# Performance work log

Hardware: AMD Instinct MI355X
Metric: run time of the kernel (lower is better)

The kernel has to match this reference:

```python
import jax, jax.numpy as jnp
import numpy as np

N = 50000
E = 800000
IN_DIM = 256
HID = 64
HEADS = 6
OUT_DIM = 32
NEG_SLOPE = 0.2


def gat_conv(x, src, dst, W, att_src, att_dst, bias, heads, ch, n_nodes):
    """PyG GATConv (eval mode): lin proj, per-edge LeakyReLU attention,
    segment softmax over destination neighborhoods, scatter-add aggregate.
    src/dst already include self-loops. Returns [n_nodes, heads, ch]."""
    h = (x @ W).reshape(n_nodes, heads, ch)            # [N,H,C]
    a_src = jnp.sum(h * att_src, axis=-1)              # [N,H]
    a_dst = jnp.sum(h * att_dst, axis=-1)              # [N,H]
    e = jax.nn.leaky_relu(a_src[src] + a_dst[dst], NEG_SLOPE)   # [E,H]
    m = jax.ops.segment_max(e, dst, num_segments=n_nodes)       # [N,H]
    ex = jnp.exp(e - m[dst])                                    # [E,H]
    denom = jax.ops.segment_sum(ex, dst, num_segments=n_nodes)  # [N,H]
    alpha = ex / denom[dst]                                     # [E,H]
    out = jax.ops.segment_sum(h[src] * alpha[:, :, None], dst, num_segments=n_nodes)
    return out + bias.reshape(1, heads, ch)


def setup_inputs() -> dict:
    key = jax.random.key(0)
    ks = jax.random.split(key, 10)
    x = jax.random.normal(ks[0], (N, IN_DIM), dtype=jnp.float32)
    edge_index = jax.random.randint(ks[1], (2, E), 0, N, dtype=jnp.int64)
    s1 = 1.0 / np.sqrt(IN_DIM)
    W1 = jax.random.normal(ks[2], (IN_DIM, HEADS * HID), dtype=jnp.float32) * s1
    att_src1 = jax.random.normal(ks[3], (1, HEADS, HID), dtype=jnp.float32) * 0.1
    att_dst1 = jax.random.normal(ks[4], (1, HEADS, HID), dtype=jnp.float32) * 0.1
    b1 = jnp.zeros((HEADS * HID,), dtype=jnp.float32)
    s2 = 1.0 / np.sqrt(HEADS * HID)
    W2 = jax.random.normal(ks[5], (HEADS * HID, OUT_DIM), dtype=jnp.float32) * s2
    att_src2 = jax.random.normal(ks[6], (1, 1, OUT_DIM), dtype=jnp.float32) * 0.1
    att_dst2 = jax.random.normal(ks[7], (1, 1, OUT_DIM), dtype=jnp.float32) * 0.1
    b2 = jnp.zeros((OUT_DIM,), dtype=jnp.float32)
    return {"x": x, "edge_index": edge_index, "W1": W1, "att_src1": att_src1,
            "att_dst1": att_dst1, "b1": b1, "W2": W2, "att_src2": att_src2,
            "att_dst2": att_dst2, "b2": b2}


def reference(x, edge_index, W1, att_src1, att_dst1, b1, W2, att_src2, att_dst2, b2):
    # PyG GATConv default add_self_loops=True
    loops = jnp.arange(N, dtype=edge_index.dtype)
    src = jnp.concatenate([edge_index[0], loops])
    dst = jnp.concatenate([edge_index[1], loops])
    h1 = gat_conv(x, src, dst, W1, att_src1, att_dst1, b1, HEADS, HID, N)
    h1 = jax.nn.relu(h1.reshape(N, HEADS * HID))  # concat=True, then ReLU; dropout = identity (eval)
    h2 = gat_conv(h1, src, dst, W2, att_src2, att_dst2, b2, 1, OUT_DIM, N)
    return h2.reshape(N, OUT_DIM)  # concat=False with 1 head == mean == squeeze
```

## Files before the change

### kernel.cpp

```cpp
#include <hip/hip_runtime.h>
#include <hip/hip_bf16.h>

#define NN 50000
#define EE 800000
#define IN_DIM 256
#define HID 64
#define HEADS 6
#define D1 384
#define OUT_DIM 32
#define NEG_SLOPE 0.2f
#define CAP 128
#define NBLK 196

typedef unsigned int uint32;
typedef unsigned short ushort_t;
typedef short short8 __attribute__((ext_vector_type(8)));
typedef float f32x4 __attribute__((ext_vector_type(4)));
typedef float f32x2 __attribute__((ext_vector_type(2)));
typedef ushort_t ushort8 __attribute__((ext_vector_type(8)));

__device__ __forceinline__ ushort_t f2bf(float f) {
    uint32 u = __builtin_bit_cast(uint32, f);
    u += 0x7fffu + ((u >> 16) & 1u);
    return (ushort_t)(u >> 16);
}
__device__ __forceinline__ float bf2f(ushort_t s) {
    uint32 u = ((uint32)s) << 16;
    return __builtin_bit_cast(float, u);
}
__device__ __forceinline__ float lo16(uint32 d) { return __builtin_bit_cast(float, d << 16); }
__device__ __forceinline__ float hi16(uint32 d) { return __builtin_bit_cast(float, d & 0xffff0000u); }


__global__ void hist_kernel(const int* __restrict__ dst, int* __restrict__ deg) {
    int i = blockIdx.x * 256 + threadIdx.x;
    if (i < EE) atomicAdd(&deg[dst[i]], 1);
}

__global__ __launch_bounds__(256) void scan1_kernel(const int* __restrict__ deg,
                                                    int* __restrict__ blockSums) {
    int t = threadIdx.x;
    int i = blockIdx.x * 256 + t;
    int v = (i < NN) ? (deg[i] + 1) : 0;
#pragma unroll
    for (int o = 32; o; o >>= 1) v += __shfl_xor(v, o);
    __shared__ int ws[4];
    if ((t & 63) == 0) ws[t >> 6] = v;
    __syncthreads();
    if (t == 0) blockSums[blockIdx.x] = ws[0] + ws[1] + ws[2] + ws[3];
}

__global__ __launch_bounds__(256) void scan2_kernel(const int* __restrict__ blockSums,
                                                    int* __restrict__ blockPrefix,
                                                    int* __restrict__ offsets) {
    int t = threadIdx.x;
    int lane = t & 63, w = t >> 6;
    int v = (t < NBLK) ? blockSums[t] : 0;
    int x = v;
#pragma unroll
    for (int o = 1; o < 64; o <<= 1) {
        int y = __shfl_up(x, o);
        if (lane >= o) x += y;
    }
    __shared__ int ws[4];
    if (lane == 63) ws[w] = x;
    __syncthreads();
    int wpre = 0;
#pragma unroll
    for (int k = 0; k < 4; ++k) if (k < w) wpre += ws[k];
    int incl = x + wpre;
    if (t < NBLK) blockPrefix[t] = incl - v;
    if (t == NBLK - 1) offsets[NN] = incl;
}

__global__ __launch_bounds__(256) void scan3_kernel(const int* __restrict__ deg,
                                                    const int* __restrict__ blockPrefix,
                                                    int* __restrict__ offsets,
                                                    int* __restrict__ cursor) {
    int t = threadIdx.x;
    int i = blockIdx.x * 256 + t;
    int lane = t & 63, w = t >> 6;
    int v = (i < NN) ? (deg[i] + 1) : 0;
    int x = v;
#pragma unroll
    for (int o = 1; o < 64; o <<= 1) {
        int y = __shfl_up(x, o);
        if (lane >= o) x += y;
    }
    __shared__ int ws[4];
    if (lane == 63) ws[w] = x;
    __syncthreads();
    int wpre = 0;
#pragma unroll
    for (int k = 0; k < 4; ++k) if (k < w) wpre += ws[k];
    int excl = x + wpre - v + blockPrefix[blockIdx.x];
    if (i < NN) { offsets[i] = excl; cursor[i] = excl; }
}

__global__ void scatter_kernel(const int* __restrict__ src, const int* __restrict__ dst,
                               int* __restrict__ cursor, int* __restrict__ srcIdx) {
    int i = blockIdx.x * 256 + threadIdx.x;
    if (i >= EE + NN) return;
    int s, d;
    if (i < EE) { s = src[i]; d = dst[i]; }
    else        { s = i - EE; d = s; }
    int pos = atomicAdd(&cursor[d], 1);
    srcIdx[pos] = s;
}


__global__ __launch_bounds__(256) void w1t_kernel(const float* __restrict__ W1,
                                                  ushort_t* __restrict__ W1Tb) {
    __shared__ float tile[32][33];
    int tx = threadIdx.x & 31, ty = threadIdx.x >> 5;
    int n0 = blockIdx.x * 32;
    int k0 = blockIdx.y * 32;
#pragma unroll
    for (int i = 0; i < 4; ++i)
        tile[ty + i * 8][tx] = W1[(k0 + ty + i * 8) * D1 + n0 + tx];
    __syncthreads();
#pragma unroll
    for (int i = 0; i < 4; ++i)
        W1Tb[(n0 + ty + i * 8) * IN_DIM + k0 + tx] = f2bf(tile[tx][ty + i * 8]);
}

__global__ __launch_bounds__(256) void w2t_kernel(const float* __restrict__ W2,
                                                  ushort_t* __restrict__ W2Tb) {
    int idx = blockIdx.x * 256 + threadIdx.x;
    if (idx < D1 * OUT_DIM) {
        int k = idx >> 5, n = idx & 31;
        W2Tb[n * D1 + k] = f2bf(W2[idx]);
    }
}


#define G1_BM 128
#define G1_BK 64

__global__ __launch_bounds__(512) void gemm1_kernel(const float* __restrict__ A,
                                                    const ushort_t* __restrict__ Bt,
                                                    const float* __restrict__ att_src,
                                                    const float* __restrict__ att_dst,
                                                    ushort_t* __restrict__ Cb,
                                                    float* __restrict__ a_src1,
                                                    float* __restrict__ a_dst1) {
    __shared__ __align__(16) ushort_t As[G1_BM][G1_BK];
    __shared__ __align__(16) ushort_t Bs[D1][G1_BK];
    __shared__ float redS[G1_BM][8];
    __shared__ float redD[G1_BM][8];
    int t = threadIdx.x;
    int m0 = blockIdx.x * G1_BM;
    int wid = t >> 6, lane = t & 63;
    int rg = wid >> 2, cg = wid & 3;
    int lrow = lane & 15, lk = lane >> 4;
    f32x4 acc[4][6] = {};
    for (int k0 = 0; k0 < IN_DIM; k0 += G1_BK) {
        {
            int r = t >> 3, c = t & 7;
#pragma unroll
            for (int p = 0; p < 2; ++p) {
                int row = p * 64 + r;
                int gr = m0 + row;
                float4 v0 = make_float4(0.f, 0.f, 0.f, 0.f), v1 = v0;
                if (gr < NN) {
                    const float* g = &A[(size_t)gr * IN_DIM + k0 + c * 8];
                    v0 = *reinterpret_cast<const float4*>(g);
                    v1 = *reinterpret_cast<const float4*>(g + 4);
                }
                ushort8 u;
                u[0] = f2bf(v0.x); u[1] = f2bf(v0.y); u[2] = f2bf(v0.z); u[3] = f2bf(v0.w);
                u[4] = f2bf(v1.x); u[5] = f2bf(v1.y); u[6] = f2bf(v1.z); u[7] = f2bf(v1.w);
                *reinterpret_cast<ushort8*>(&As[row][(c ^ (row & 7)) * 8]) = u;
            }
        }
        {
            int r = t >> 3, c = t & 7;
#pragma unroll
            for (int p = 0; p < 6; ++p) {
                int row = p * 64 + r;
                ushort8 u = *reinterpret_cast<const ushort8*>(&Bt[row * IN_DIM + k0 + c * 8]);
                *reinterpret_cast<ushort8*>(&Bs[row][(c ^ (row & 7)) * 8]) = u;
            }
        }
        __syncthreads();
#pragma unroll
        for (int kk = 0; kk < G1_BK; kk += 32) {
            int ckb = (kk >> 3) + lk;
            short8 af[4];
#pragma unroll
            for (int fm = 0; fm < 4; ++fm) {
                int m = rg * 64 + fm * 16 + lrow;
                af[fm] = *reinterpret_cast<const short8*>(&As[m][(ckb ^ (m & 7)) * 8]);
            }
#pragma unroll
            for (int fn = 0; fn < 6; ++fn) {
                int n = cg * 96 + fn * 16 + lrow;
                short8 bfv = *reinterpret_cast<const short8*>(&Bs[n][(ckb ^ (n & 7)) * 8]);
#pragma unroll
                for (int fm = 0; fm < 4; ++fm)
                    acc[fm][fn] = __builtin_amdgcn_mfma_f32_16x16x32_bf16(af[fm], bfv, acc[fm][fn], 0, 0, 0);
            }
        }
        __syncthreads();
    }
    float atS[6], atD[6];
#pragma unroll
    for (int fn = 0; fn < 6; ++fn) {
        int col = cg * 96 + fn * 16 + lrow;
        atS[fn] = att_src[col];
        atD[fn] = att_dst[col];
    }
    int split = (cg & 1) ? 2 : 4;
#pragma unroll
    for (int fm = 0; fm < 4; ++fm) {
#pragma unroll
        for (int r = 0; r < 4; ++r) {
            int rowl = rg * 64 + fm * 16 + lk * 4 + r;
            int row = m0 + rowl;
            float vsA = 0.f, vsB = 0.f, vdA = 0.f, vdB = 0.f;
#pragma unroll
            for (int fn = 0; fn < 6; ++fn) {
                float v = acc[fm][fn][r];
                if (fn < split) { vsA += v * atS[fn]; vdA += v * atD[fn]; }
                else            { vsB += v * atS[fn]; vdB += v * atD[fn]; }
            }
#pragma unroll
            for (int o = 8; o; o >>= 1) {
                vsA += __shfl_xor(vsA, o); vsB += __shfl_xor(vsB, o);
                vdA += __shfl_xor(vdA, o); vdB += __shfl_xor(vdB, o);
            }
            if (lrow == 0) {
                redS[rowl][cg * 2 + 0] = vsA; redS[rowl][cg * 2 + 1] = vsB;
                redD[rowl][cg * 2 + 0] = vdA; redD[rowl][cg * 2 + 1] = vdB;
            }
            if (row < NN) {
#pragma unroll
                for (int fn = 0; fn < 6; ++fn) {
                    int col = cg * 96 + fn * 16 + lrow;
                    Cb[(size_t)row * D1 + col] = f2bf(acc[fm][fn][r]);
                }
            }
        }
    }
    __syncthreads();
    if (t < G1_BM) {
        int row = m0 + t;
        if (row < NN) {
            float s0 = redS[t][0], s1 = redS[t][1] + redS[t][2], s2 = redS[t][3];
            float s3 = redS[t][4], s4 = redS[t][5] + redS[t][6], s5 = redS[t][7];
            float d0 = redD[t][0], d1 = redD[t][1] + redD[t][2], d2 = redD[t][3];
            float d3 = redD[t][4], d4 = redD[t][5] + redD[t][6], d5 = redD[t][7];
            float* ps = &a_src1[(size_t)row * HEADS];
            float* pd = &a_dst1[(size_t)row * HEADS];
            ps[0] = s0; ps[1] = s1; ps[2] = s2; ps[3] = s3; ps[4] = s4; ps[5] = s5;
            pd[0] = d0; pd[1] = d1; pd[2] = d2; pd[3] = d3; pd[4] = d4; pd[5] = d5;
        }
    }
}


__global__ __launch_bounds__(256, 4) void agg1_kernel(const uint32* __restrict__ H1d,
                                                      const float* __restrict__ a_src,
                                                      const float* __restrict__ a_dst,
                                                      const int* __restrict__ offsets,
                                                      const int* __restrict__ srcIdx,
                                                      const float* __restrict__ b1,
                                                      uint32* __restrict__ out1d) {
    __shared__ float pl[4][HEADS][CAP + 1];
    __shared__ int   sl[4][CAP];
    int w = threadIdx.x >> 6, lane = threadIdx.x & 63;
    int hb = lane >> 5;
    int n = blockIdx.x * 4 + w;
    const float2* asv = (const float2*)a_src;
    float ad[HEADS];
#pragma unroll
    for (int h = 0; h < HEADS; ++h) ad[h] = a_dst[n * HEADS + h];
    float ldn[HEADS] = {0.f, 0.f, 0.f, 0.f, 0.f, 0.f};
    float acc[6] = {0.f, 0.f, 0.f, 0.f, 0.f, 0.f};
    int beg = offsets[n], end = offsets[n + 1];
    for (int cbeg = beg; cbeg < end; cbeg += CAP) {
        int L = end - cbeg; if (L > CAP) L = CAP;
        for (int tI = lane; tI < L; tI += 64) {
            int s = srcIdx[cbeg + tI];
            sl[w][tI] = s;
            float2 e0 = asv[s * 3 + 0];
            float2 e1 = asv[s * 3 + 1];
            float2 e2 = asv[s * 3 + 2];
            float ev[6] = {e0.x, e0.y, e1.x, e1.y, e2.x, e2.y};
#pragma unroll
            for (int h = 0; h < HEADS; ++h) {
                float e = ev[h] + ad[h];
                e = e > 0.f ? e : NEG_SLOPE * e;
                float p = __expf(e);
                pl[w][h][tI] = p;
                ldn[h] += p;
            }
        }
        int j = 0;
        for (; j + 4 <= L; j += 4) {
            int s0 = sl[w][j], s1 = sl[w][j + 1], s2 = sl[w][j + 2], s3 = sl[w][j + 3];
            const uint32* h0 = H1d + (size_t)s0 * 192 + lane;
            const uint32* h1 = H1d + (size_t)s1 * 192 + lane;
            const uint32* h2 = H1d + (size_t)s2 * 192 + lane;
            const uint32* h3 = H1d + (size_t)s3 * 192 + lane;
            uint32 a0 = h0[0], a1 = h0[64], a2 = h0[128];
            uint32 b0 = h1[0], b1v_ = h1[64], b2 = h1[128];
            uint32 c0 = h2[0], c1 = h2[64], c2 = h2[128];
            uint32 d0 = h3[0], d1 = h3[64], d2 = h3[128];
            float p00 = pl[w][hb][j],     p01 = pl[w][2 + hb][j],     p02 = pl[w][4 + hb][j];
            float p10 = pl[w][hb][j + 1], p11 = pl[w][2 + hb][j + 1], p12 = pl[w][4 + hb][j + 1];
            float p20 = pl[w][hb][j + 2], p21 = pl[w][2 + hb][j + 2], p22 = pl[w][4 + hb][j + 2];
            float p30 = pl[w][hb][j + 3], p31 = pl[w][2 + hb][j + 3], p32 = pl[w][4 + hb][j + 3];
            acc[0] += p00 * lo16(a0); acc[1] += p00 * hi16(a0);
            acc[2] += p01 * lo16(a1); acc[3] += p01 * hi16(a1);
            acc[4] += p02 * lo16(a2); acc[5] += p02 * hi16(a2);
            acc[0] += p10 * lo16(b0); acc[1] += p10 * hi16(b0);
            acc[2] += p11 * lo16(b1v_); acc[3] += p11 * hi16(b1v_);
            acc[4] += p12 * lo16(b2); acc[5] += p12 * hi16(b2);
            acc[0] += p20 * lo16(c0); acc[1] += p20 * hi16(c0);
            acc[2] += p21 * lo16(c1); acc[3] += p21 * hi16(c1);
            acc[4] += p22 * lo16(c2); acc[5] += p22 * hi16(c2);
            acc[0] += p30 * lo16(d0); acc[1] += p30 * hi16(d0);
            acc[2] += p31 * lo16(d1); acc[3] += p31 * hi16(d1);
            acc[4] += p32 * lo16(d2); acc[5] += p32 * hi16(d2);
        }
        for (; j < L; ++j) {
            int s0 = sl[w][j];
            const uint32* h0 = H1d + (size_t)s0 * 192 + lane;
            uint32 x0 = h0[0], x1 = h0[64], x2 = h0[128];
            float p0 = pl[w][hb][j], p1 = pl[w][2 + hb][j], p2 = pl[w][4 + hb][j];
            acc[0] += p0 * lo16(x0); acc[1] += p0 * hi16(x0);
            acc[2] += p1 * lo16(x1); acc[3] += p1 * hi16(x1);
            acc[4] += p2 * lo16(x2); acc[5] += p2 * hi16(x2);
        }
    }
#pragma unroll
    for (int h = 0; h < HEADS; ++h) {
#pragma unroll
        for (int o = 32; o; o >>= 1) ldn[h] += __shfl_xor(ldn[h], o);
    }
    float dsel[3];
#pragma unroll
    for (int k = 0; k < 3; ++k) dsel[k] = hb ? ldn[2 * k + 1] : ldn[2 * k];
    const float2* b1v = (const float2*)b1;
#pragma unroll
    for (int k = 0; k < 3; ++k) {
        float2 bb = b1v[k * 64 + lane];
        float v0 = fmaxf(acc[2 * k]     / dsel[k] + bb.x, 0.f);
        float v1 = fmaxf(acc[2 * k + 1] / dsel[k] + bb.y, 0.f);
        uint32 pk = (uint32)f2bf(v0) | ((uint32)f2bf(v1) << 16);
        __builtin_nontemporal_store(pk, &out1d[(size_t)n * 192 + k * 64 + lane]);
    }
}


#define G2_ROWS 256

__global__ __launch_bounds__(256) void gemm2_kernel(const ushort_t* __restrict__ Xb,
                                                    const ushort_t* __restrict__ W2Tb,
                                                    const float* __restrict__ att_src2,
                                                    const float* __restrict__ att_dst2,
                                                    ushort_t* __restrict__ H2b,
                                                    float* __restrict__ a_src2,
                                                    float* __restrict__ a_dst2) {
    __shared__ __align__(16) ushort_t Ws[OUT_DIM][D1];
    __shared__ __align__(16) ushort_t Xs[G2_ROWS][64];
    int t = threadIdx.x;
    int wid = t >> 6, lane = t & 63;
    int lrow = lane & 15, lk = lane >> 4;
    int m0 = blockIdx.x * G2_ROWS;
#pragma unroll
    for (int p = 0; p < 6; ++p) {
        int chunk = p * 256 + t;
        int nr = chunk / 48, c = chunk % 48;
        ushort8 u = *reinterpret_cast<const ushort8*>(&W2Tb[nr * D1 + c * 8]);
        int span = c >> 3, cc = c & 7;
        *reinterpret_cast<ushort8*>(&Ws[nr][(cc ^ (nr & 7)) * 8 + span * 64]) = u;
    }
    f32x4 acc[4][2] = {};
    for (int kc = 0; kc < 6; ++kc) {
        int k0 = kc * 64;
        {
            int r = t >> 3, c = t & 7;
#pragma unroll
            for (int p = 0; p < 8; ++p) {
                int row = p * 32 + r;
                int gr = m0 + row;
                ushort8 u = {0, 0, 0, 0, 0, 0, 0, 0};
                if (gr < NN) u = *reinterpret_cast<const ushort8*>(&Xb[(size_t)gr * D1 + k0 + c * 8]);
                *reinterpret_cast<ushort8*>(&Xs[row][(c ^ (row & 7)) * 8]) = u;
            }
        }
        __syncthreads();
#pragma unroll
        for (int kk = 0; kk < 64; kk += 32) {
            int ckb = (kk >> 3) + lk;
            short8 af[4];
#pragma unroll
            for (int fm = 0; fm < 4; ++fm) {
                int mm = wid * 64 + fm * 16 + lrow;
                af[fm] = *reinterpret_cast<const short8*>(&Xs[mm][(ckb ^ (mm & 7)) * 8]);
            }
#pragma unroll
            for (int fn = 0; fn < 2; ++fn) {
                int nn2 = fn * 16 + lrow;
                short8 bfv = *reinterpret_cast<const short8*>(&Ws[nn2][(ckb ^ (nn2 & 7)) * 8 + kc * 64]);
#pragma unroll
                for (int fm = 0; fm < 4; ++fm)
                    acc[fm][fn] = __builtin_amdgcn_mfma_f32_16x16x32_bf16(af[fm], bfv, acc[fm][fn], 0, 0, 0);
            }
        }
        __syncthreads();
    }
    float as2a = att_src2[lrow], as2b = att_src2[16 + lrow];
    float ad2a = att_dst2[lrow], ad2b = att_dst2[16 + lrow];
#pragma unroll
    for (int fm = 0; fm < 4; ++fm) {
#pragma unroll
        for (int r = 0; r < 4; ++r) {
            int row = m0 + wid * 64 + fm * 16 + lk * 4 + r;
            float h0 = acc[fm][0][r], h1 = acc[fm][1][r];
            float vs = h0 * as2a + h1 * as2b;
            float vd = h0 * ad2a + h1 * ad2b;
#pragma unroll
            for (int o = 8; o; o >>= 1) {
                vs += __shfl_xor(vs, o);
                vd += __shfl_xor(vd, o);
            }
            if (row < NN) {
                H2b[(size_t)row * OUT_DIM + lrow]      = f2bf(h0);
                H2b[(size_t)row * OUT_DIM + 16 + lrow] = f2bf(h1);
                if (lrow == 0) { a_src2[row] = vs; a_dst2[row] = vd; }
            }
        }
    }
}


__global__ __launch_bounds__(256, 4) void agg2_kernel(const ushort_t* __restrict__ H2b,
                                                      const float* __restrict__ a_src,
                                                      const float* __restrict__ a_dst,
                                                      const int* __restrict__ offsets,
                                                      const int* __restrict__ srcIdx,
                                                      const float* __restrict__ b2,
                                                      float* __restrict__ out) {
    __shared__ float pl[4][CAP];
    __shared__ int   sl[4][CAP];
    int w = threadIdx.x >> 6, lane = threadIdx.x & 63;
    int n = blockIdx.x * 4 + w;
    int q = lane & 15, par = lane >> 4;
    const uint32* H2d = (const uint32*)H2b;
    float ad = a_dst[n];
    float ldn = 0.f, ax = 0.f, ay = 0.f;
    int beg = offsets[n], end = offsets[n + 1];
    for (int cbeg = beg; cbeg < end; cbeg += CAP) {
        int L = end - cbeg; if (L > CAP) L = CAP;
        for (int tI = lane; tI < L; tI += 64) {
            int s = srcIdx[cbeg + tI];
            sl[w][tI] = s;
            float e = a_src[s] + ad;
            e = e > 0.f ? e : NEG_SLOPE * e;
            float p = __expf(e);
            pl[w][tI] = p;
            ldn += p;
        }
        int j = 0;
        for (; j + 8 <= L; j += 8) {
            int s0 = sl[w][j + par], s1 = sl[w][j + 4 + par];
            float p0 = pl[w][j + par], p1 = pl[w][j + 4 + par];
            uint32 d0 = H2d[(size_t)s0 * 16 + q];
            uint32 d1 = H2d[(size_t)s1 * 16 + q];
            ax += p0 * lo16(d0) + p1 * lo16(d1);
            ay += p0 * hi16(d0) + p1 * hi16(d1);
        }
        for (; j < L; j += 4) {
            int jj = j + par;
            if (jj < L) {
                int s = sl[w][jj];
                float p = pl[w][jj];
                uint32 d = H2d[(size_t)s * 16 + q];
                ax += p * lo16(d);
                ay += p * hi16(d);
            }
        }
    }
#pragma unroll
    for (int o = 32; o; o >>= 1) ldn += __shfl_xor(ldn, o);
    ax += __shfl_xor(ax, 16); ax += __shfl_xor(ax, 32);
    ay += __shfl_xor(ay, 16); ay += __shfl_xor(ay, 32);
    if (lane < 16) {
        float2 bb = ((const float2*)b2)[q];
        f32x2 o;
        o[0] = ax / ldn + bb.x;
        o[1] = ay / ldn + bb.y;
        __builtin_nontemporal_store(o, (f32x2*)&out[(size_t)n * 32 + q * 2]);
    }
}


static inline size_t align256(size_t x) { return (x + 255) & ~size_t(255); }

extern "C" void kernel_launch(void* const* d_in, const int* in_sizes, int n_in,
                              void* d_out, int out_size, void* d_ws, size_t ws_size,
                              hipStream_t stream) {
    const float* x        = (const float*)d_in[0];
    const int*   ei       = (const int*)d_in[1];
    const float* W1       = (const float*)d_in[2];
    const float* att_src1 = (const float*)d_in[3];
    const float* att_dst1 = (const float*)d_in[4];
    const float* b1       = (const float*)d_in[5];
    const float* W2       = (const float*)d_in[6];
    const float* att_src2 = (const float*)d_in[7];
    const float* att_dst2 = (const float*)d_in[8];
    const float* b2       = (const float*)d_in[9];
    float* out = (float*)d_out;

    const int* e_src = ei;
    const int* e_dst = ei + EE;

    char* p = (char*)d_ws;
    ushort_t* H1b   = (ushort_t*)p; p += align256(sizeof(ushort_t) * (size_t)NN * D1);
    ushort_t* OUT1b = (ushort_t*)p; p += align256(sizeof(ushort_t) * (size_t)NN * D1);
    ushort_t* H2b   = (ushort_t*)p; p += align256(sizeof(ushort_t) * (size_t)NN * OUT_DIM);
    ushort_t* W1Tb  = (ushort_t*)p; p += align256(sizeof(ushort_t) * D1 * IN_DIM);
    ushort_t* W2Tb  = (ushort_t*)p; p += align256(sizeof(ushort_t) * D1 * OUT_DIM);
    float* AS1  = (float*)p; p += align256(sizeof(float) * NN * HEADS);
    float* AD1  = (float*)p; p += align256(sizeof(float) * NN * HEADS);
    float* AS2  = (float*)p; p += align256(sizeof(float) * NN);
    float* AD2  = (float*)p; p += align256(sizeof(float) * NN);
    int*   DEG  = (int*)p;   p += align256(sizeof(int) * NN);
    int*   OFF  = (int*)p;   p += align256(sizeof(int) * (NN + 1));
    int*   CUR  = (int*)p;   p += align256(sizeof(int) * NN);
    int*   BSUM = (int*)p;   p += align256(sizeof(int) * NBLK);
    int*   BPRE = (int*)p;   p += align256(sizeof(int) * NBLK);
    int*   SIDX = (int*)p;   p += align256(sizeof(int) * (EE + NN));

    (void)hipMemsetAsync(DEG, 0, sizeof(int) * NN, stream);
    w1t_kernel<<<dim3(D1 / 32, IN_DIM / 32), 256, 0, stream>>>(W1, W1Tb);
    w2t_kernel<<<48, 256, 0, stream>>>(W2, W2Tb);
    hist_kernel<<<(EE + 255) / 256, 256, 0, stream>>>(e_dst, DEG);
    scan1_kernel<<<NBLK, 256, 0, stream>>>(DEG, BSUM);
    scan2_kernel<<<1, 256, 0, stream>>>(BSUM, BPRE, OFF);
    scan3_kernel<<<NBLK, 256, 0, stream>>>(DEG, BPRE, OFF, CUR);
    scatter_kernel<<<(EE + NN + 255) / 256, 256, 0, stream>>>(e_src, e_dst, CUR, SIDX);

    gemm1_kernel<<<(NN + G1_BM - 1) / G1_BM, 512, 0, stream>>>(x, W1Tb, att_src1, att_dst1, H1b, AS1, AD1);
    agg1_kernel<<<NN / 4, 256, 0, stream>>>((const uint32*)H1b, AS1, AD1, OFF, SIDX, b1, (uint32*)OUT1b);

    gemm2_kernel<<<(NN + G2_ROWS - 1) / G2_ROWS, 256, 0, stream>>>(OUT1b, W2Tb, att_src2, att_dst2, H2b, AS2, AD2);
    agg2_kernel<<<NN / 4, 256, 0, stream>>>(H2b, AS2, AD2, OFF, SIDX, b2, out);
}
```

Before: 316.5 us.

## Fuse layer-2 projection into agg1 epilogue and merge prep kernels

Each agg1 wavefront now stages its aggregated bf16 row in shared memory and computes that node's 32-wide layer-2 projection with scalar dot products against W2T. It also produces the a_src2/a_dst2 attention terms, which removes the separate MFMA gemm2 kernel and the 38 MB OUT1 round trip through HBM. The W1/W2 transposes and the degree zeroing are merged into one prep kernel to cut launches. In exchange, agg1 does 384-long FMA loops per lane with W2T read from global/L1, adds shared memory and a block barrier, and may lose occupancy.

```diff
diff --git a/kernel.cpp b/kernel.cpp
--- a/kernel.cpp
+++ b/kernel.cpp
@@ -32,6 +32,37 @@
 __device__ __forceinline__ float hi16(uint32 d) { return __builtin_bit_cast(float, d & 0xffff0000u); }
 
 
+__global__ __launch_bounds__(256) void prep_kernel(const float* __restrict__ W1,
+                                                   ushort_t* __restrict__ W1Tb,
+                                                   const float* __restrict__ W2,
+                                                   ushort_t* __restrict__ W2Tb,
+                                                   int* __restrict__ deg) {
+    int bx = blockIdx.x;
+    if (bx < 96) {
+        __shared__ float tile[32][33];
+        int tx = threadIdx.x & 31, ty = threadIdx.x >> 5;
+        int n0 = (bx % 12) * 32;
+        int k0 = (bx / 12) * 32;
+#pragma unroll
+        for (int i = 0; i < 4; ++i)
+            tile[ty + i * 8][tx] = W1[(k0 + ty + i * 8) * D1 + n0 + tx];
+        __syncthreads();
+#pragma unroll
+        for (int i = 0; i < 4; ++i)
+            W1Tb[(n0 + ty + i * 8) * IN_DIM + k0 + tx] = f2bf(tile[tx][ty + i * 8]);
+    } else if (bx < 144) {
+        int idx = (bx - 96) * 256 + threadIdx.x;
+        if (idx < D1 * OUT_DIM) {
+            int k = idx >> 5, n = idx & 31;
+            W2Tb[n * D1 + k] = f2bf(W2[idx]);
+        }
+    } else {
+        int i = (bx - 144) * 256 + threadIdx.x;
+        if (i < NN) deg[i] = 0;
+    }
+}
+
+
 __global__ void hist_kernel(const int* __restrict__ dst, int* __restrict__ deg) {
     int i = blockIdx.x * 256 + threadIdx.x;
     if (i < EE) atomicAdd(&deg[dst[i]], 1);
@@ -106,31 +137,6 @@
     else        { s = i - EE; d = s; }
     int pos = atomicAdd(&cursor[d], 1);
     srcIdx[pos] = s;
-}
-
-
-__global__ __launch_bounds__(256) void w1t_kernel(const float* __restrict__ W1,
-                                                  ushort_t* __restrict__ W1Tb) {
-    __shared__ float tile[32][33];
-    int tx = threadIdx.x & 31, ty = threadIdx.x >> 5;
-    int n0 = blockIdx.x * 32;
-    int k0 = blockIdx.y * 32;
-#pragma unroll
-    for (int i = 0; i < 4; ++i)
-        tile[ty + i * 8][tx] = W1[(k0 + ty + i * 8) * D1 + n0 + tx];
-    __syncthreads();
-#pragma unroll
-    for (int i = 0; i < 4; ++i)
-        W1Tb[(n0 + ty + i * 8) * IN_DIM + k0 + tx] = f2bf(tile[tx][ty + i * 8]);
-}
-
-__global__ __launch_bounds__(256) void w2t_kernel(const float* __restrict__ W2,
-                                                  ushort_t* __restrict__ W2Tb) {
-    int idx = blockIdx.x * 256 + threadIdx.x;
-    if (idx < D1 * OUT_DIM) {
-        int k = idx >> 5, n = idx & 31;
-        W2Tb[n * D1 + k] = f2bf(W2[idx]);
-    }
 }
 
 
@@ -265,9 +271,15 @@
                                                       const int* __restrict__ offsets,
                                                       const int* __restrict__ srcIdx,
                                                       const float* __restrict__ b1,
-                                                      uint32* __restrict__ out1d) {
+                                                      const ushort_t* __restrict__ W2Tb,
+                                                      const float* __restrict__ att_src2,
+                                                      const float* __restrict__ att_dst2,
+                                                      ushort_t* __restrict__ H2b,
+                                                      float* __restrict__ a_src2,
+                                                      float* __restrict__ a_dst2) {
     __shared__ float pl[4][HEADS][CAP + 1];
     __shared__ int   sl[4][CAP];
+    __shared__ uint32 rowbuf[4][192];
     int w = threadIdx.x >> 6, lane = threadIdx.x & 63;
     int hb = lane >> 5;
     int n = blockIdx.x * 4 + w;
@@ -348,92 +360,29 @@
         float2 bb = b1v[k * 64 + lane];
         float v0 = fmaxf(acc[2 * k]     / dsel[k] + bb.x, 0.f);
         float v1 = fmaxf(acc[2 * k + 1] / dsel[k] + bb.y, 0.f);
-        uint32 pk = (uint32)f2bf(v0) | ((uint32)f2bf(v1) << 16);
-        __builtin_nontemporal_store(pk, &out1d[(size_t)n * 192 + k * 64 + lane]);
-    }
-}
-
-
-#define G2_ROWS 256
-
-__global__ __launch_bounds__(256) void gemm2_kernel(const ushort_t* __restrict__ Xb,
-                                                    const ushort_t* __restrict__ W2Tb,
-                                                    const float* __restrict__ att_src2,
-                                                    const float* __restrict__ att_dst2,
-                                                    ushort_t* __restrict__ H2b,
-                                                    float* __restrict__ a_src2,
-                                                    float* __restrict__ a_dst2) {
-    __shared__ __align__(16) ushort_t Ws[OUT_DIM][D1];
-    __shared__ __align__(16) ushort_t Xs[G2_ROWS][64];
-    int t = threadIdx.x;
-    int wid = t >> 6, lane = t & 63;
-    int lrow = lane & 15, lk = lane >> 4;
-    int m0 = blockIdx.x * G2_ROWS;
-#pragma unroll
-    for (int p = 0; p < 6; ++p) {
-        int chunk = p * 256 + t;
-        int nr = chunk / 48, c = chunk % 48;
-        ushort8 u = *reinterpret_cast<const ushort8*>(&W2Tb[nr * D1 + c * 8]);
-        int span = c >> 3, cc = c & 7;
-        *reinterpret_cast<ushort8*>(&Ws[nr][(cc ^ (nr & 7)) * 8 + span * 64]) = u;
-    }
-    f32x4 acc[4][2] = {};
-    for (int kc = 0; kc < 6; ++kc) {
-        int k0 = kc * 64;
-        {
-            int r = t >> 3, c = t & 7;
-#pragma unroll
-            for (int p = 0; p < 8; ++p) {
-                int row = p * 32 + r;
-                int gr = m0 + row;
-                ushort8 u = {0, 0, 0, 0, 0, 0, 0, 0};
-                if (gr < NN) u = *reinterpret_cast<const ushort8*>(&Xb[(size_t)gr * D1 + k0 + c * 8]);
-                *reinterpret_cast<ushort8*>(&Xs[row][(c ^ (row & 7)) * 8]) = u;
-            }
-        }
-        __syncthreads();
-#pragma unroll
-        for (int kk = 0; kk < 64; kk += 32) {
-            int ckb = (kk >> 3) + lk;
-            short8 af[4];
-#pragma unroll
-            for (int fm = 0; fm < 4; ++fm) {
-                int mm = wid * 64 + fm * 16 + lrow;
-                af[fm] = *reinterpret_cast<const short8*>(&Xs[mm][(ckb ^ (mm & 7)) * 8]);
-            }
-#pragma unroll
-            for (int fn = 0; fn < 2; ++fn) {
-                int nn2 = fn * 16 + lrow;
-                short8 bfv = *reinterpret_cast<const short8*>(&Ws[nn2][(ckb ^ (nn2 & 7)) * 8 + kc * 64]);
-#pragma unroll
-                for (int fm = 0; fm < 4; ++fm)
-                    acc[fm][fn] = __builtin_amdgcn_mfma_f32_16x16x32_bf16(af[fm], bfv, acc[fm][fn], 0, 0, 0);
-            }
-        }
-        __syncthreads();
-    }
-    float as2a = att_src2[lrow], as2b = att_src2[16 + lrow];
-    float ad2a = att_dst2[lrow], ad2b = att_dst2[16 + lrow];
-#pragma unroll
-    for (int fm = 0; fm < 4; ++fm) {
-#pragma unroll
-        for (int r = 0; r < 4; ++r) {
-            int row = m0 + wid * 64 + fm * 16 + lk * 4 + r;
-            float h0 = acc[fm][0][r], h1 = acc[fm][1][r];
-            float vs = h0 * as2a + h1 * as2b;
-            float vd = h0 * ad2a + h1 * ad2b;
-#pragma unroll
-            for (int o = 8; o; o >>= 1) {
-                vs += __shfl_xor(vs, o);
-                vd += __shfl_xor(vd, o);
-            }
-            if (row < NN) {
-                H2b[(size_t)row * OUT_DIM + lrow]      = f2bf(h0);
-                H2b[(size_t)row * OUT_DIM + 16 + lrow] = f2bf(h1);
-                if (lrow == 0) { a_src2[row] = vs; a_dst2[row] = vd; }
-            }
-        }
-    }
+        rowbuf[w][k * 64 + lane] = (uint32)f2bf(v0) | ((uint32)f2bf(v1) << 16);
+    }
+    __syncthreads();
+    int c = lane & 31, half = lane >> 5;
+    const uint32* w2d = (const uint32*)W2Tb + c * 192 + half * 96;
+    const uint32* rb = &rowbuf[w][half * 96];
+    float hacc = 0.f;
+#pragma unroll 8
+    for (int j = 0; j < 96; ++j) {
+        uint32 rw = rb[j];
+        uint32 ww = w2d[j];
+        hacc += lo16(rw) * lo16(ww) + hi16(rw) * hi16(ww);
+    }
+    hacc += __shfl_xor(hacc, 32);
+    float vs = hacc * att_src2[c];
+    float vd = hacc * att_dst2[c];
+#pragma unroll
+    for (int o = 16; o; o >>= 1) {
+        vs += __shfl_xor(vs, o);
+        vd += __shfl_xor(vd, o);
+    }
+    if (lane < 32) H2b[(size_t)n * OUT_DIM + c] = f2bf(hacc);
+    if (lane == 0) { a_src2[n] = vs; a_dst2[n] = vd; }
 }
 
 
@@ -520,7 +469,6 @@
 
     char* p = (char*)d_ws;
     ushort_t* H1b   = (ushort_t*)p; p += align256(sizeof(ushort_t) * (size_t)NN * D1);
-    ushort_t* OUT1b = (ushort_t*)p; p += align256(sizeof(ushort_t) * (size_t)NN * D1);
     ushort_t* H2b   = (ushort_t*)p; p += align256(sizeof(ushort_t) * (size_t)NN * OUT_DIM);
     ushort_t* W1Tb  = (ushort_t*)p; p += align256(sizeof(ushort_t) * D1 * IN_DIM);
     ushort_t* W2Tb  = (ushort_t*)p; p += align256(sizeof(ushort_t) * D1 * OUT_DIM);
@@ -535,9 +483,7 @@
     int*   BPRE = (int*)p;   p += align256(sizeof(int) * NBLK);
     int*   SIDX = (int*)p;   p += align256(sizeof(int) * (EE + NN));
 
-    (void)hipMemsetAsync(DEG, 0, sizeof(int) * NN, stream);
-    w1t_kernel<<<dim3(D1 / 32, IN_DIM / 32), 256, 0, stream>>>(W1, W1Tb);
-    w2t_kernel<<<48, 256, 0, stream>>>(W2, W2Tb);
+    prep_kernel<<<340, 256, 0, stream>>>(W1, W1Tb, W2, W2Tb, DEG);
     hist_kernel<<<(EE + 255) / 256, 256, 0, stream>>>(e_dst, DEG);
     scan1_kernel<<<NBLK, 256, 0, stream>>>(DEG, BSUM);
     scan2_kernel<<<1, 256, 0, stream>>>(BSUM, BPRE, OFF);
@@ -545,8 +491,8 @@
     scatter_kernel<<<(EE + NN + 255) / 256, 256, 0, stream>>>(e_src, e_dst, CUR, SIDX);
 
     gemm1_kernel<<<(NN + G1_BM - 1) / G1_BM, 512, 0, stream>>>(x, W1Tb, att_src1, att_dst1, H1b, AS1, AD1);
-    agg1_kernel<<<NN / 4, 256, 0, stream>>>((const uint32*)H1b, AS1, AD1, OFF, SIDX, b1, (uint32*)OUT1b);
-
-    gemm2_kernel<<<(NN + G2_ROWS - 1) / G2_ROWS, 256, 0, stream>>>(OUT1b, W2Tb, att_src2, att_dst2, H2b, AS2, AD2);
+    agg1_kernel<<<NN / 4, 256, 0, stream>>>((const uint32*)H1b, AS1, AD1, OFF, SIDX, b1,
+                                            W2Tb, att_src2, att_dst2, H2b, AS2, AD2);
+
     agg2_kernel<<<NN / 4, 256, 0, stream>>>(H2b, AS2, AD2, OFF, SIDX, b2, out);
 }
```

Measured after the change: 364.9 us. +15.3%, slower.
